# Performance work log

Measured on AMD Instinct MI355X. Metric: run time of the kernel, lower is better.

Reference implementation:

```python
import jax, jax.numpy as jnp
import numpy as np

N = 100_000   # nodes
E = 1_600_000 # edges (avg degree 16)
B = 512       # graphs in batch
F_IN = 64; H = 4; D = 64; HD = H * D; EXTRA = 16
NEG_SLOPE = 0.2  # DGL GATConv default


def _gat_conv(x, src, dst, W, al, ar, bias):
    """DGL GATConv: fc -> per-head attn logits -> edge leaky_relu -> segment softmax over dst -> scatter-sum."""
    h = (x @ W).reshape(N, H, D)                       # [N,H,D]
    el = jnp.sum(h * al, axis=-1)                      # [N,H]
    er = jnp.sum(h * ar, axis=-1)                      # [N,H]
    e = jax.nn.leaky_relu(el[src] + er[dst], NEG_SLOPE)  # [E,H]
    m = jax.ops.segment_max(e, dst, num_segments=N)    # [N,H]
    m = jnp.where(jnp.isfinite(m), m, 0.0)             # guard empty segments
    ex = jnp.exp(e - m[dst])                           # [E,H]
    den = jax.ops.segment_sum(ex, dst, num_segments=N) # [N,H]
    alpha = ex / jnp.maximum(den[dst], 1e-9)           # [E,H]
    msg = h[src] * alpha[:, :, None]                   # [E,H,D]
    out = jax.ops.segment_sum(msg, dst, num_segments=N) + bias.reshape(1, H, D)
    return out  # [N,H,D]


def setup_inputs() -> dict:
    key = jax.random.key(0)
    ks = jax.random.split(key, 26)
    nrm = lambda k, shape: jax.random.normal(k, shape, dtype=jnp.float32) * 0.5
    src = jax.random.randint(ks[0], (E,), 0, N)
    # ensure every node has >=1 incoming edge (DGL disallows zero in-degree by default)
    dst = jnp.concatenate([jnp.arange(N), jax.random.randint(ks[1], (E - N,), 0, N)])
    node_graph = jnp.sort(jax.random.randint(ks[2], (N,), 0, B))
    inp = dict(
        src=src, dst=dst, node_graph=node_graph,
        feats_node=jax.random.normal(ks[3], (N, F_IN), dtype=jnp.float32),
        feats_graph=jax.random.normal(ks[4], (B, EXTRA), dtype=jnp.float32),
        W1=nrm(ks[5], (F_IN, HD)), al1=nrm(ks[6], (H, D)), ar1=nrm(ks[7], (H, D)), bg1=jnp.zeros(HD),
        W2=nrm(ks[8], (HD, HD)),  al2=nrm(ks[9], (H, D)), ar2=nrm(ks[10], (H, D)), bg2=jnp.zeros(HD),
        W3=nrm(ks[11], (HD, HD)), al3=nrm(ks[12], (H, D)), ar3=nrm(ks[13], (H, D)), bg3=jnp.zeros(HD),
        sw=nrm(ks[14], (HD, 1)), sb=jnp.zeros(1),
        lw1=nrm(ks[15], (HD + EXTRA, 2 * D)), lb1=jnp.zeros(2 * D),
        lw2=nrm(ks[16], (2 * D, D)), lb2=jnp.zeros(D),
        lw3=nrm(ks[17], (D, 1)), lb3=jnp.zeros(1),
    )
    return inp


def reference(src, dst, node_graph, feats_node, feats_graph,
              W1, al1, ar1, bg1, W2, al2, ar2, bg2, W3, al3, ar3, bg3,
              sw, sb, lw1, lb1, lw2, lb2, lw3, lb3):
    selu = jax.nn.selu
    x = selu(_gat_conv(feats_node, src, dst, W1, al1, ar1, bg1)).reshape(N, HD)
    x = selu(_gat_conv(x, src, dst, W2, al2, ar2, bg2)).reshape(N, HD)
    x = selu(_gat_conv(x, src, dst, W3, al3, ar3, bg3)).reshape(N, HD)
    # WeightedAverage readout: sigmoid-scored weighted mean per graph
    w = jax.nn.sigmoid(x @ sw + sb)                               # [N,1]
    num = jax.ops.segment_sum(w * x, node_graph, num_segments=B)  # [B,HD]
    den = jax.ops.segment_sum(w, node_graph, num_segments=B)      # [B,1]
    emb = num / jnp.maximum(den, 1e-9)
    y = jnp.concatenate([emb, feats_graph], axis=1)
    y = selu(y @ lw1 + lb1)
    y = selu(y @ lw2 + lb2)
    return y @ lw3 + lb3  # [B,1]
```

## Files before the change

kernel.cpp:

```cpp
#include <hip/hip_runtime.h>

#define N_NODES 100000
#define N_EDGES 1600000
#define N_GRAPHS 512
#define F_IN 64
#define HD 256
#define EXTRA 16
#define SCAN_BLOCK 512

typedef float f32x4 __attribute__((ext_vector_type(4)));
typedef _Float16 f16x4 __attribute__((ext_vector_type(4)));
typedef _Float16 f16x8 __attribute__((ext_vector_type(8)));

__device__ __forceinline__ float selu_f(float x) {
    const float a = 1.6732632423543772f, sc = 1.0507009873554805f;
    return x > 0.f ? sc * x : sc * a * (__expf(x) - 1.f);
}

__global__ __launch_bounds__(256) void hist_k(const int* __restrict__ dst, int* __restrict__ hist) {
    int j = blockIdx.x * 256 + threadIdx.x;
    if (j < N_EDGES) atomicAdd(&hist[dst[j]], 1);
}

__global__ __launch_bounds__(SCAN_BLOCK) void scan1_k(const int* __restrict__ hist,
                                                      int* __restrict__ row_ptr,
                                                      int* __restrict__ bsums) {
    __shared__ int sm[SCAN_BLOCK];
    int t = threadIdx.x;
    int i = blockIdx.x * SCAN_BLOCK + t;
    int v = (i < N_NODES) ? hist[i] : 0;
    sm[t] = v;
    __syncthreads();
    for (int off = 1; off < SCAN_BLOCK; off <<= 1) {
        int add = (t >= off) ? sm[t - off] : 0;
        __syncthreads();
        sm[t] += add;
        __syncthreads();
    }
    if (i < N_NODES) row_ptr[i] = sm[t] - v;
    if (t == SCAN_BLOCK - 1) bsums[blockIdx.x] = sm[t];
}

__global__ __launch_bounds__(256) void scan23_k(int* __restrict__ row_ptr, const int* __restrict__ bsums,
                                                int* __restrict__ cursor, int nb) {
    __shared__ int bs[256];
    int t = threadIdx.x;
    bs[t] = (t < nb) ? bsums[t] : 0;
    __syncthreads();
    for (int off = 1; off < 256; off <<= 1) {
        int add = (t >= off) ? bs[t - off] : 0;
        __syncthreads();
        bs[t] += add;
        __syncthreads();
    }
    int i = blockIdx.x * 256 + t;
    if (i < N_NODES) {
        int b = i / SCAN_BLOCK;
        int p = b > 0 ? bs[b - 1] : 0;
        int r = row_ptr[i] + p;
        row_ptr[i] = r;
        cursor[i] = r;
    }
    if (i == 0) row_ptr[N_NODES] = N_EDGES;
}

__global__ __launch_bounds__(256) void scatter_k(const int* __restrict__ src,
                                                 const int* __restrict__ dst,
                                                 int* __restrict__ cursor,
                                                 int* __restrict__ csr_src) {
    int j = blockIdx.x * 256 + threadIdx.x;
    if (j < N_EDGES) {
        int r = atomicAdd(&cursor[dst[j]], 1);
        r = r < N_EDGES ? r : N_EDGES - 1;
        csr_src[r] = src[j];
    }
}

__device__ __forceinline__ void wsplit(const float* __restrict__ W, _Float16* __restrict__ Wh,
                                       _Float16* __restrict__ Wl, int idx, int K) {
    int n = idx / K, k = idx - n * K;
    float w = W[(size_t)k * HD + n];
    _Float16 hi = (_Float16)w;
    Wh[idx] = hi;
    Wl[idx] = (_Float16)(w - (float)hi);
}

__global__ __launch_bounds__(256) void prep_k(const float* __restrict__ W1,
                                              const float* __restrict__ W2,
                                              const float* __restrict__ W3,
                                              _Float16* __restrict__ W1h, _Float16* __restrict__ W1l,
                                              _Float16* __restrict__ W2h, _Float16* __restrict__ W2l,
                                              _Float16* __restrict__ W3h, _Float16* __restrict__ W3l,
                                              const int* __restrict__ node_graph,
                                              int* __restrict__ gstart) {
    int b = blockIdx.x, t = threadIdx.x;
    if (b < 64) {
        wsplit(W1, W1h, W1l, b * 256 + t, F_IN);
    } else if (b < 320) {
        wsplit(W2, W2h, W2l, (b - 64) * 256 + t, HD);
    } else if (b < 576) {
        wsplit(W3, W3h, W3l, (b - 320) * 256 + t, HD);
    } else {
        int g = (b - 576) * 256 + t;
        if (g > N_GRAPHS) return;
        int lo = 0, hi = N_NODES;
        while (lo < hi) {
            int mid = (lo + hi) >> 1;
            if (node_graph[mid] < g) lo = mid + 1; else hi = mid;
        }
        gstart[g] = lo;
    }
}

template <int K, bool F32A, int ATERMS>
__global__ __launch_bounds__(256) void gemm_split_k(const void* __restrict__ Aptr,
                                                    const _Float16* __restrict__ Alo_p,
                                                    const _Float16* __restrict__ Bt_hi,
                                                    const _Float16* __restrict__ Bt_lo,
                                                    const float* __restrict__ al,
                                                    const float* __restrict__ ar,
                                                    _Float16* __restrict__ Chi,
                                                    float* __restrict__ el,
                                                    float* __restrict__ er, int M) {
    const int BM = 64, BN = 128, LDP = 40;
    __shared__ union {
        struct {
            _Float16 Ash[BM][LDP];
            _Float16 Asl[BM][LDP];
            _Float16 Bsh[BN][LDP];
            _Float16 Bsl[BN][LDP];
        } s;
        _Float16 ctile[BM][BN];
    } u;
    __shared__ float pl[4][64];
    __shared__ float pr[4][64];
    _Float16 (&Ash)[BM][LDP] = u.s.Ash;
    _Float16 (&Asl)[BM][LDP] = u.s.Asl;
    _Float16 (&Bsh)[BN][LDP] = u.s.Bsh;
    _Float16 (&Bsl)[BN][LDP] = u.s.Bsl;

    int tid = threadIdx.x;
    int w = tid >> 6, lane = tid & 63;
    int q = lane >> 4, l16 = lane & 15;
    int row0 = blockIdx.y * BM, col0 = blockIdx.x * BN;
    f32x4 acc[4][2] = {};

    int ar_ = tid >> 2, ao = (tid & 3) * 8;
    f16x8 rAh, rAl, rBh[2], rBl[2];

    auto load_tile = [&](int k0) {
        int gr = row0 + ar_;
        if constexpr (F32A) {
            const float* A32 = (const float*)Aptr;
            float vv[8] = {};
            if (gr < M) {
                float4 va = *(const float4*)(A32 + (size_t)gr * K + k0 + ao);
                float4 vb = *(const float4*)(A32 + (size_t)gr * K + k0 + ao + 4);
                vv[0] = va.x; vv[1] = va.y; vv[2] = va.z; vv[3] = va.w;
                vv[4] = vb.x; vv[5] = vb.y; vv[6] = vb.z; vv[7] = vb.w;
            }
            f16x8 h, l;
#pragma unroll
            for (int i = 0; i < 8; i++) {
                h[i] = (_Float16)vv[i];
                l[i] = (_Float16)(vv[i] - (float)h[i]);
            }
            rAh = h; rAl = l;
        } else {
            const _Float16* Ahi = (const _Float16*)Aptr;
            f16x8 vh = {};
            if (gr < M) {
                vh = *(const f16x8*)(Ahi + (size_t)gr * K + k0 + ao);
                if constexpr (ATERMS == 3) rAl = *(const f16x8*)(Alo_p + (size_t)gr * K + k0 + ao);
            } else if constexpr (ATERMS == 3) {
                rAl = f16x8{};
            }
            rAh = vh;
        }
#pragma unroll
        for (int c = 0; c < 2; c++) {
            int cc = tid + c * 256;
            int br = cc >> 2, bo = (cc & 3) * 8;
            int gb = col0 + br;
            rBh[c] = *(const f16x8*)(Bt_hi + (size_t)gb * K + k0 + bo);
            rBl[c] = *(const f16x8*)(Bt_lo + (size_t)gb * K + k0 + bo);
        }
    };
    auto store_tile = [&]() {
        *(f16x8*)&Ash[ar_][ao] = rAh;
        if constexpr (ATERMS == 3) *(f16x8*)&Asl[ar_][ao] = rAl;
#pragma unroll
        for (int c = 0; c < 2; c++) {
            int cc = tid + c * 256;
            int br = cc >> 2, bo = (cc & 3) * 8;
            *(f16x8*)&Bsh[br][bo] = rBh[c];
            *(f16x8*)&Bsl[br][bo] = rBl[c];
        }
    };

    load_tile(0);
    store_tile();
    __syncthreads();

    for (int k0 = 0; k0 < K; k0 += 32) {
        bool more = (k0 + 32) < K;
        if (more) load_tile(k0 + 32);

        f16x8 ah[4], alo2[4], bh[2], bl[2];
#pragma unroll
        for (int mf = 0; mf < 4; mf++) {
            int m = mf * 16 + l16;
            ah[mf] = *(const f16x8*)&Ash[m][q * 8];
            if constexpr (ATERMS == 3) alo2[mf] = *(const f16x8*)&Asl[m][q * 8];
        }
#pragma unroll
        for (int nf = 0; nf < 2; nf++) {
            int n = w * 32 + nf * 16 + l16;
            bh[nf] = *(const f16x8*)&Bsh[n][q * 8];
            bl[nf] = *(const f16x8*)&Bsl[n][q * 8];
        }
#pragma unroll
        for (int mf = 0; mf < 4; mf++)
#pragma unroll
            for (int nf = 0; nf < 2; nf++) {
                acc[mf][nf] = __builtin_amdgcn_mfma_f32_16x16x32_f16(ah[mf], bh[nf], acc[mf][nf], 0, 0, 0);
                acc[mf][nf] = __builtin_amdgcn_mfma_f32_16x16x32_f16(ah[mf], bl[nf], acc[mf][nf], 0, 0, 0);
                if constexpr (ATERMS == 3)
                    acc[mf][nf] = __builtin_amdgcn_mfma_f32_16x16x32_f16(alo2[mf], bh[nf], acc[mf][nf], 0, 0, 0);
            }
        if (more) {
            __syncthreads();
            store_tile();
            __syncthreads();
        }
    }

    __syncthreads();

    const int hh = (col0 >> 6) + (w >> 1);
    float alv[2], arv[2];
#pragma unroll
    for (int nf = 0; nf < 2; nf++) {
        int d = (w & 1) * 32 + nf * 16 + l16;
        alv[nf] = al[hh * 64 + d];
        arv[nf] = ar[hh * 64 + d];
    }
#pragma unroll
    for (int mf = 0; mf < 4; mf++) {
#pragma unroll
        for (int i = 0; i < 4; i++) {
            int rl = mf * 16 + q * 4 + i;
            float e_l = 0.f, e_r = 0.f;
#pragma unroll
            for (int nf = 0; nf < 2; nf++) {
                float v = acc[mf][nf][i];
                u.ctile[rl][w * 32 + nf * 16 + l16] = (_Float16)v;
                e_l = fmaf(v, alv[nf], e_l);
                e_r = fmaf(v, arv[nf], e_r);
            }
#pragma unroll
            for (int off = 1; off < 16; off <<= 1) {
                e_l += __shfl_xor(e_l, off, 64);
                e_r += __shfl_xor(e_r, off, 64);
            }
            if (l16 == 0) {
                pl[w][rl] = e_l;
                pr[w][rl] = e_r;
            }
        }
    }
    __syncthreads();
#pragma unroll
    for (int j = 0; j < 4; j++) {
        int c = tid + j * 256;
        int rr2 = c >> 4, co = (c & 15) * 8;
        int gr = row0 + rr2;
        if (gr < M)
            *(f16x8*)(Chi + (size_t)gr * HD + col0 + co) = *(const f16x8*)&u.ctile[rr2][co];
    }
    int h2 = (tid >> 6) & 1, rr = tid & 63;
    int grow = row0 + rr;
    if (grow < M) {
        if (tid < 128) el[(size_t)grow * 4 + (col0 >> 6) + h2] = pl[2 * h2][rr] + pl[2 * h2 + 1][rr];
        else           er[(size_t)grow * 4 + (col0 >> 6) + h2] = pr[2 * h2][rr] + pr[2 * h2 + 1][rr];
    }
}

template <int OUT>
__global__ __launch_bounds__(256) void gat_aggregate_k(const _Float16* __restrict__ hb,
                                                       const float* __restrict__ el,
                                                       const float* __restrict__ er,
                                                       const int* __restrict__ csr_src,
                                                       const int* __restrict__ row_ptr,
                                                       const float* __restrict__ bias,
                                                       _Float16* __restrict__ xhi,
                                                       const float* __restrict__ sw,
                                                       const float* __restrict__ sb,
                                                       float* __restrict__ wsc) {
    __shared__ float wlds[4][64][4];
    __shared__ int snlds[4][64];
    int wv = threadIdx.x >> 6;
    int lane = threadIdx.x & 63;
    int v = blockIdx.x * 4 + wv;
    bool valid = v < N_NODES;
    int vc = valid ? v : 0;
    int rs = row_ptr[vc];
    int deg = valid ? row_ptr[vc + 1] - rs : 0;
    float4 erv = make_float4(0.f, 0.f, 0.f, 0.f);
    if (valid) erv = *(const float4*)(er + (size_t)vc * 4);

    const int eo = lane >> 5;
    const int fl = lane & 31;
    const int headf = fl >> 3;

    float a[8] = {};
    float dw = 0.f;
    float m_h = 0.f, er_h = 0.f;

    if (deg <= 64) {
        float e0 = -1e30f, e1 = -1e30f, e2 = -1e30f, e3 = -1e30f;
        int my_sn = 0;
        if (lane < deg) {
            my_sn = csr_src[rs + lane];
            float4 elv = *(const float4*)(el + (size_t)my_sn * 4);
            float t0 = elv.x + erv.x, t1 = elv.y + erv.y, t2 = elv.z + erv.z, t3 = elv.w + erv.w;
            e0 = t0 > 0.f ? t0 : 0.2f * t0;
            e1 = t1 > 0.f ? t1 : 0.2f * t1;
            e2 = t2 > 0.f ? t2 : 0.2f * t2;
            e3 = t3 > 0.f ? t3 : 0.2f * t3;
        }
        int P = (deg + 1) >> 1;
        f16x8 hv[8];
        int pA = P < 4 ? P : 4;
#pragma unroll
        for (int u = 0; u < 4; u++) {
            if (u < pA) {
                int idx = 2 * u + eo;
                int cidx = idx < deg ? idx : deg - 1;
                int snb = __shfl(my_sn, cidx, 64);
                hv[u] = *(const f16x8*)(hb + (size_t)snb * HD + fl * 8);
            }
        }
        float m0 = e0, m1 = e1, m2 = e2, m3 = e3;
        for (int off = 1; off < deg; off <<= 1) {
            m0 = fmaxf(m0, __shfl_xor(m0, off, 64));
            m1 = fmaxf(m1, __shfl_xor(m1, off, 64));
            m2 = fmaxf(m2, __shfl_xor(m2, off, 64));
            m3 = fmaxf(m3, __shfl_xor(m3, off, 64));
        }
        if (lane < deg) {
            wlds[wv][lane][0] = __expf(e0 - m0);
            wlds[wv][lane][1] = __expf(e1 - m1);
            wlds[wv][lane][2] = __expf(e2 - m2);
            wlds[wv][lane][3] = __expf(e3 - m3);
            snlds[wv][lane] = my_sn;
        }

        int pB = P < 8 ? P : 8;
#pragma unroll
        for (int u = 4; u < 8; u++) {
            if (u < pB) {
                int idx = 2 * u + eo;
                int cidx = idx < deg ? idx : deg - 1;
                hv[u] = *(const f16x8*)(hb + (size_t)snlds[wv][cidx] * HD + fl * 8);
            }
        }
        for (int pb = 0; pb < P; pb += 8) {
#pragma unroll
            for (int j = 0; j < 8; j++) {
                int p = pb + j;
                if (p >= P) break;
                int idx = 2 * p + eo;
                float w = (idx < deg) ? wlds[wv][idx][headf] : 0.f;
                dw += w;
                f16x8 h = hv[j];
#pragma unroll
                for (int i = 0; i < 8; i++) a[i] = fmaf(w, (float)h[i], a[i]);
                int pn = p + 8;
                if (pn < P) {
                    int idx2 = 2 * pn + eo;
                    int cidx2 = idx2 < deg ? idx2 : deg - 1;
                    hv[j] = *(const f16x8*)(hb + (size_t)snlds[wv][cidx2] * HD + fl * 8);
                }
            }
        }
    } else {
        float m[4] = {-1e30f, -1e30f, -1e30f, -1e30f};
        float s[4] = {0.f, 0.f, 0.f, 0.f};
        for (int t = lane; t < deg; t += 64) {
            int sn = csr_src[rs + t];
            float4 elv = *(const float4*)(el + (size_t)sn * 4);
            float e[4];
            e[0] = elv.x + erv.x; e[1] = elv.y + erv.y; e[2] = elv.z + erv.z; e[3] = elv.w + erv.w;
#pragma unroll
            for (int hh = 0; hh < 4; hh++) {
                float ev = e[hh] > 0.f ? e[hh] : 0.2f * e[hh];
                float mn = fmaxf(m[hh], ev);
                s[hh] = s[hh] * __expf(m[hh] - mn) + __expf(ev - mn);
                m[hh] = mn;
            }
        }
#pragma unroll
        for (int off = 32; off >= 1; off >>= 1) {
#pragma unroll
            for (int hh = 0; hh < 4; hh++) {
                float mo = __shfl_xor(m[hh], off, 64);
                float so = __shfl_xor(s[hh], off, 64);
                float mn = fmaxf(m[hh], mo);
                s[hh] = s[hh] * __expf(m[hh] - mn) + so * __expf(mo - mn);
                m[hh] = mn;
            }
        }
        m_h = headf == 0 ? m[0] : headf == 1 ? m[1] : headf == 2 ? m[2] : m[3];
        float dh = headf == 0 ? s[0] : headf == 1 ? s[1] : headf == 2 ? s[2] : s[3];
        er_h = headf == 0 ? erv.x : headf == 1 ? erv.y : headf == 2 ? erv.z : erv.w;
        dw = (eo == 0) ? dh : 0.f;

        for (int t = 0; t < deg; t += 2) {
            int idx = t + eo;
            int cidx = idx < deg ? idx : idx - 1;
            int sn = csr_src[rs + cidx];
            float w = 0.f;
            if (idx < deg) {
                float e = el[(size_t)sn * 4 + headf] + er_h;
                e = e > 0.f ? e : 0.2f * e;
                w = __expf(e - m_h);
            }
            f16x8 hv = *(const f16x8*)(hb + (size_t)sn * HD + fl * 8);
#pragma unroll
            for (int i = 0; i < 8; i++) a[i] = fmaf(w, (float)hv[i], a[i]);
        }
    }

#pragma unroll
    for (int i = 0; i < 8; i++) a[i] += __shfl_xor(a[i], 32, 64);
    dw += __shfl_xor(dw, 32, 64);
    float inv_den = 1.f / fmaxf(dw, 1e-9f);

    float4 bv0 = *(const float4*)(bias + fl * 8);
    float4 bv1 = *(const float4*)(bias + fl * 8 + 4);
    float o[8];
    o[0] = selu_f(fmaf(a[0], inv_den, bv0.x));
    o[1] = selu_f(fmaf(a[1], inv_den, bv0.y));
    o[2] = selu_f(fmaf(a[2], inv_den, bv0.z));
    o[3] = selu_f(fmaf(a[3], inv_den, bv0.w));
    o[4] = selu_f(fmaf(a[4], inv_den, bv1.x));
    o[5] = selu_f(fmaf(a[5], inv_den, bv1.y));
    o[6] = selu_f(fmaf(a[6], inv_den, bv1.z));
    o[7] = selu_f(fmaf(a[7], inv_den, bv1.w));

    if constexpr (OUT == 0) {
        if (valid && eo == 0) {
            f16x8 oh;
#pragma unroll
            for (int i = 0; i < 8; i++) oh[i] = (_Float16)o[i];
            *(f16x8*)(xhi + (size_t)v * HD + fl * 8) = oh;
        }
    } else {
        float p;
        if (eo == 0) {
            if (valid) {
                f16x4 oh;
                oh.x = (_Float16)o[0]; oh.y = (_Float16)o[1];
                oh.z = (_Float16)o[2]; oh.w = (_Float16)o[3];
                *(f16x4*)(xhi + (size_t)v * HD + fl * 8) = oh;
            }
            float4 sv = *(const float4*)(sw + fl * 8);
            p = o[0] * sv.x + o[1] * sv.y + o[2] * sv.z + o[3] * sv.w;
        } else {
            if (valid) {
                f16x4 oh;
                oh.x = (_Float16)o[4]; oh.y = (_Float16)o[5];
                oh.z = (_Float16)o[6]; oh.w = (_Float16)o[7];
                *(f16x4*)(xhi + (size_t)v * HD + fl * 8 + 4) = oh;
            }
            float4 sv = *(const float4*)(sw + fl * 8 + 4);
            p = o[4] * sv.x + o[5] * sv.y + o[6] * sv.z + o[7] * sv.w;
        }
#pragma unroll
        for (int off = 1; off < 64; off <<= 1) p += __shfl_xor(p, off, 64);
        if (lane == 0 && valid) wsc[v] = 1.f / (1.f + __expf(-(p + sb[0])));
    }
}

__global__ __launch_bounds__(256) void readout_part_k(const _Float16* __restrict__ x,
                                                      const float* __restrict__ wsc,
                                                      const int* __restrict__ gstart,
                                                      float* __restrict__ y0p) {
    int g = blockIdx.x >> 2, c = blockIdx.x & 3;
    int f = threadIdx.x;
    int s0 = gstart[g], e0 = gstart[g + 1];
    int len = e0 - s0;
    int cs = s0 + (len * c) / 4, ce = s0 + (len * (c + 1)) / 4;
    float num = 0.f, den = 0.f;
#pragma unroll 4
    for (int n = cs; n < ce; n++) {
        float wn = wsc[n];
        num = fmaf(wn, (float)x[(size_t)n * HD + f], num);
        den += wn;
    }
    float* dst = y0p + (size_t)(g * 4 + c) * 257;
    dst[f] = num;
    if (f == 0) dst[256] = den;
}

__global__ __launch_bounds__(128) void mlp_k(const float* __restrict__ y0p,
                                             const float* __restrict__ fg,
                                             const float* __restrict__ lw1, const float* __restrict__ lb1,
                                             const float* __restrict__ lw2, const float* __restrict__ lb2,
                                             const float* __restrict__ lw3, const float* __restrict__ lb3,
                                             float* __restrict__ out) {
    __shared__ float y0s[272];
    __shared__ float y1s[128];
    int g = blockIdx.x, t = threadIdx.x;
    const float* p0 = y0p + (size_t)(g * 4 + 0) * 257;
    const float* p1 = y0p + (size_t)(g * 4 + 1) * 257;
    const float* p2 = y0p + (size_t)(g * 4 + 2) * 257;
    const float* p3 = y0p + (size_t)(g * 4 + 3) * 257;
    float den = p0[256] + p1[256] + p2[256] + p3[256];
    float invden = 1.f / fmaxf(den, 1e-9f);
    for (int i = t; i < 256; i += 128)
        y0s[i] = (p0[i] + p1[i] + p2[i] + p3[i]) * invden;
    if (t < EXTRA) y0s[256 + t] = fg[g * EXTRA + t];
    __syncthreads();
    float acc = lb1[t];
    for (int k = 0; k < 272; k++) acc = fmaf(y0s[k], lw1[k * 128 + t], acc);
    y1s[t] = selu_f(acc);
    __syncthreads();
    if (t < 64) {
        float a2 = lb2[t];
        for (int k = 0; k < 128; k++) a2 = fmaf(y1s[k], lw2[k * 64 + t], a2);
        float v2 = selu_f(a2);
        float p = v2 * lw3[t];
#pragma unroll
        for (int off = 1; off < 64; off <<= 1) p += __shfl_xor(p, off, 64);
        if (t == 0) out[g] = p + lb3[0];
    }
}

extern "C" void kernel_launch(void* const* d_in, const int* in_sizes, int n_in,
                              void* d_out, int out_size, void* d_ws, size_t ws_size,
                              hipStream_t stream) {
    const int* src = (const int*)d_in[0];
    const int* dst = (const int*)d_in[1];
    const int* node_graph = (const int*)d_in[2];
    const float* feats_node = (const float*)d_in[3];
    const float* feats_graph = (const float*)d_in[4];
    const float* W1 = (const float*)d_in[5];
    const float* al1 = (const float*)d_in[6];
    const float* ar1 = (const float*)d_in[7];
    const float* bg1 = (const float*)d_in[8];
    const float* W2 = (const float*)d_in[9];
    const float* al2 = (const float*)d_in[10];
    const float* ar2 = (const float*)d_in[11];
    const float* bg2 = (const float*)d_in[12];
    const float* W3 = (const float*)d_in[13];
    const float* al3 = (const float*)d_in[14];
    const float* ar3 = (const float*)d_in[15];
    const float* bg3 = (const float*)d_in[16];
    const float* sw = (const float*)d_in[17];
    const float* sb = (const float*)d_in[18];
    const float* lw1 = (const float*)d_in[19];
    const float* lb1 = (const float*)d_in[20];
    const float* lw2 = (const float*)d_in[21];
    const float* lb2 = (const float*)d_in[22];
    const float* lw3 = (const float*)d_in[23];
    const float* lb3 = (const float*)d_in[24];
    float* out = (float*)d_out;

    char* ws = (char*)d_ws;
    size_t off = 0;
    auto alloc = [&](size_t bytes) -> char* {
        char* p = ws + off;
        off += (bytes + 255) & ~(size_t)255;
        return p;
    };
    _Float16* xhi = (_Float16*)alloc((size_t)N_NODES * HD * 2);
    _Float16* hhi = (_Float16*)alloc((size_t)N_NODES * HD * 2);
    _Float16* W1hi = (_Float16*)alloc((size_t)F_IN * HD * 2);
    _Float16* W1lo = (_Float16*)alloc((size_t)F_IN * HD * 2);
    _Float16* W2hi = (_Float16*)alloc((size_t)HD * HD * 2);
    _Float16* W2lo = (_Float16*)alloc((size_t)HD * HD * 2);
    _Float16* W3hi = (_Float16*)alloc((size_t)HD * HD * 2);
    _Float16* W3lo = (_Float16*)alloc((size_t)HD * HD * 2);
    float* el = (float*)alloc((size_t)N_NODES * 4 * 4);
    float* er = (float*)alloc((size_t)N_NODES * 4 * 4);
    float* wsc = (float*)alloc((size_t)N_NODES * 4);
    float* y0p = (float*)alloc((size_t)N_GRAPHS * 4 * 257 * 4);
    int* hist = (int*)alloc((size_t)N_NODES * 4);
    int* row_ptr = (int*)alloc((size_t)(N_NODES + 1) * 4);
    int* cursor = (int*)alloc((size_t)N_NODES * 4);
    int* csr_src = (int*)alloc((size_t)N_EDGES * 4);
    int* gstart = (int*)alloc((size_t)(N_GRAPHS + 1) * 4);
    int* bsums = (int*)alloc(256 * 4);
    (void)ws_size; (void)in_sizes; (void)n_in; (void)out_size;

    hipMemsetAsync(hist, 0, (size_t)N_NODES * 4, stream);

    hist_k<<<(N_EDGES + 255) / 256, 256, 0, stream>>>(dst, hist);
    int nb = (N_NODES + SCAN_BLOCK - 1) / SCAN_BLOCK;
    scan1_k<<<nb, SCAN_BLOCK, 0, stream>>>(hist, row_ptr, bsums);
    scan23_k<<<(N_NODES + 255) / 256, 256, 0, stream>>>(row_ptr, bsums, cursor, nb);
    scatter_k<<<(N_EDGES + 255) / 256, 256, 0, stream>>>(src, dst, cursor, csr_src);

    prep_k<<<579, 256, 0, stream>>>(W1, W2, W3, W1hi, W1lo, W2hi, W2lo, W3hi, W3lo, node_graph, gstart);

    dim3 ggrid(HD / 128, (N_NODES + 63) / 64);
    int nwb = (N_NODES + 3) / 4;

    gemm_split_k<F_IN, true, 3><<<ggrid, 256, 0, stream>>>((const void*)feats_node, nullptr, W1hi, W1lo, al1, ar1, hhi, el, er, N_NODES);
    gat_aggregate_k<0><<<nwb, 256, 0, stream>>>(hhi, el, er, csr_src, row_ptr, bg1, xhi, nullptr, nullptr, nullptr);
    gemm_split_k<HD, false, 2><<<ggrid, 256, 0, stream>>>((const void*)xhi, nullptr, W2hi, W2lo, al2, ar2, hhi, el, er, N_NODES);
    gat_aggregate_k<0><<<nwb, 256, 0, stream>>>(hhi, el, er, csr_src, row_ptr, bg2, xhi, nullptr, nullptr, nullptr);
    gemm_split_k<HD, false, 2><<<ggrid, 256, 0, stream>>>((const void*)xhi, nullptr, W3hi, W3lo, al3, ar3, hhi, el, er, N_NODES);
    gat_aggregate_k<1><<<nwb, 256, 0, stream>>>(hhi, el, er, csr_src, row_ptr, bg3, xhi, sw, sb, wsc);

    readout_part_k<<<N_GRAPHS * 4, 256, 0, stream>>>(xhi, wsc, gstart, y0p);
    mlp_k<<<N_GRAPHS, 128, 0, stream>>>(y0p, feats_graph, lw1, lb1, lw2, lb2, lw3, lb3, out);
}
```

Measured before the change: 882.8 us.

## Merge CSR build kernels with weight prep and first GEMM via block-range dispatch

The edge histogram is folded into the weight-split/gstart prep kernel, and the CSR scatter is folded into the first-layer GEMM kernel. Each merged kernel decides its role from blockIdx ranges. This removes two launches and lets independent work share the GPU, so the atomic-bound scatter can overlap with the GEMM compute. The risks are that block scheduling order puts the edge blocks first, which limits the overlap, and that the merged kernel's register and LDS usage is set by the GEMM body, which may lower occupancy for the scatter blocks.

Result: slower. 907.9 us (+2.8%).

```diff
diff --git a/kernel.cpp b/kernel.cpp
--- a/kernel.cpp
+++ b/kernel.cpp
@@ -7,6 +7,7 @@
 #define HD 256
 #define EXTRA 16
 #define SCAN_BLOCK 512
+#define EDGE_BLOCKS 6250
 
 typedef float f32x4 __attribute__((ext_vector_type(4)));
 typedef _Float16 f16x4 __attribute__((ext_vector_type(4)));
@@ -15,11 +16,6 @@
 __device__ __forceinline__ float selu_f(float x) {
     const float a = 1.6732632423543772f, sc = 1.0507009873554805f;
     return x > 0.f ? sc * x : sc * a * (__expf(x) - 1.f);
-}
-
-__global__ __launch_bounds__(256) void hist_k(const int* __restrict__ dst, int* __restrict__ hist) {
-    int j = blockIdx.x * 256 + threadIdx.x;
-    if (j < N_EDGES) atomicAdd(&hist[dst[j]], 1);
 }
 
 __global__ __launch_bounds__(SCAN_BLOCK) void scan1_k(const int* __restrict__ hist,
@@ -64,18 +60,6 @@
     if (i == 0) row_ptr[N_NODES] = N_EDGES;
 }
 
-__global__ __launch_bounds__(256) void scatter_k(const int* __restrict__ src,
-                                                 const int* __restrict__ dst,
-                                                 int* __restrict__ cursor,
-                                                 int* __restrict__ csr_src) {
-    int j = blockIdx.x * 256 + threadIdx.x;
-    if (j < N_EDGES) {
-        int r = atomicAdd(&cursor[dst[j]], 1);
-        r = r < N_EDGES ? r : N_EDGES - 1;
-        csr_src[r] = src[j];
-    }
-}
-
 __device__ __forceinline__ void wsplit(const float* __restrict__ W, _Float16* __restrict__ Wh,
                                        _Float16* __restrict__ Wl, int idx, int K) {
     int n = idx / K, k = idx - n * K;
@@ -85,15 +69,22 @@
     Wl[idx] = (_Float16)(w - (float)hi);
 }
 
-__global__ __launch_bounds__(256) void prep_k(const float* __restrict__ W1,
-                                              const float* __restrict__ W2,
-                                              const float* __restrict__ W3,
-                                              _Float16* __restrict__ W1h, _Float16* __restrict__ W1l,
-                                              _Float16* __restrict__ W2h, _Float16* __restrict__ W2l,
-                                              _Float16* __restrict__ W3h, _Float16* __restrict__ W3l,
-                                              const int* __restrict__ node_graph,
-                                              int* __restrict__ gstart) {
-    int b = blockIdx.x, t = threadIdx.x;
+__global__ __launch_bounds__(256) void histprep_k(const int* __restrict__ dst, int* __restrict__ hist,
+                                                  const float* __restrict__ W1,
+                                                  const float* __restrict__ W2,
+                                                  const float* __restrict__ W3,
+                                                  _Float16* __restrict__ W1h, _Float16* __restrict__ W1l,
+                                                  _Float16* __restrict__ W2h, _Float16* __restrict__ W2l,
+                                                  _Float16* __restrict__ W3h, _Float16* __restrict__ W3l,
+                                                  const int* __restrict__ node_graph,
+                                                  int* __restrict__ gstart) {
+    int bid = blockIdx.x, t = threadIdx.x;
+    if (bid < EDGE_BLOCKS) {
+        int j = bid * 256 + t;
+        if (j < N_EDGES) atomicAdd(&hist[dst[j]], 1);
+        return;
+    }
+    int b = bid - EDGE_BLOCKS;
     if (b < 64) {
         wsplit(W1, W1h, W1l, b * 256 + t, F_IN);
     } else if (b < 320) {
@@ -113,17 +104,18 @@
 }
 
 template <int K, bool F32A, int ATERMS>
-__global__ __launch_bounds__(256) void gemm_split_k(const void* __restrict__ Aptr,
-                                                    const _Float16* __restrict__ Alo_p,
-                                                    const _Float16* __restrict__ Bt_hi,
-                                                    const _Float16* __restrict__ Bt_lo,
-                                                    const float* __restrict__ al,
-                                                    const float* __restrict__ ar,
-                                                    _Float16* __restrict__ Chi,
-                                                    float* __restrict__ el,
-                                                    float* __restrict__ er, int M) {
+__device__ __forceinline__ void gemm_body(int bx, int by,
+                                          const void* __restrict__ Aptr,
+                                          const _Float16* __restrict__ Alo_p,
+                                          const _Float16* __restrict__ Bt_hi,
+                                          const _Float16* __restrict__ Bt_lo,
+                                          const float* __restrict__ al,
+                                          const float* __restrict__ ar,
+                                          _Float16* __restrict__ Chi,
+                                          float* __restrict__ el,
+                                          float* __restrict__ er, int M) {
     const int BM = 64, BN = 128, LDP = 40;
-    __shared__ union {
+    __shared__ union U {
         struct {
             _Float16 Ash[BM][LDP];
             _Float16 Asl[BM][LDP];
@@ -142,7 +134,7 @@
     int tid = threadIdx.x;
     int w = tid >> 6, lane = tid & 63;
     int q = lane >> 4, l16 = lane & 15;
-    int row0 = blockIdx.y * BM, col0 = blockIdx.x * BN;
+    int row0 = by * BM, col0 = bx * BN;
     f32x4 acc[4][2] = {};
 
     int ar_ = tid >> 2, ao = (tid & 3) * 8;
@@ -284,6 +276,46 @@
         if (tid < 128) el[(size_t)grow * 4 + (col0 >> 6) + h2] = pl[2 * h2][rr] + pl[2 * h2 + 1][rr];
         else           er[(size_t)grow * 4 + (col0 >> 6) + h2] = pr[2 * h2][rr] + pr[2 * h2 + 1][rr];
     }
+}
+
+template <int K, bool F32A, int ATERMS>
+__global__ __launch_bounds__(256) void gemm_k(const void* __restrict__ Aptr,
+                                              const _Float16* __restrict__ Alo_p,
+                                              const _Float16* __restrict__ Bt_hi,
+                                              const _Float16* __restrict__ Bt_lo,
+                                              const float* __restrict__ al,
+                                              const float* __restrict__ ar,
+                                              _Float16* __restrict__ Chi,
+                                              float* __restrict__ el,
+                                              float* __restrict__ er, int M) {
+    gemm_body<K, F32A, ATERMS>(blockIdx.x, blockIdx.y, Aptr, Alo_p, Bt_hi, Bt_lo, al, ar, Chi, el, er, M);
+}
+
+__global__ __launch_bounds__(256) void mega1_k(const int* __restrict__ src,
+                                               const int* __restrict__ dst,
+                                               int* __restrict__ cursor,
+                                               int* __restrict__ csr_src,
+                                               const float* __restrict__ feats_node,
+                                               const _Float16* __restrict__ W1h,
+                                               const _Float16* __restrict__ W1l,
+                                               const float* __restrict__ al1,
+                                               const float* __restrict__ ar1,
+                                               _Float16* __restrict__ hhi,
+                                               float* __restrict__ el,
+                                               float* __restrict__ er) {
+    int bid = blockIdx.x;
+    if (bid < EDGE_BLOCKS) {
+        int j = bid * 256 + threadIdx.x;
+        if (j < N_EDGES) {
+            int r = atomicAdd(&cursor[dst[j]], 1);
+            r = r < N_EDGES ? r : N_EDGES - 1;
+            csr_src[r] = src[j];
+        }
+        return;
+    }
+    int g = bid - EDGE_BLOCKS;
+    gemm_body<F_IN, true, 3>(g & 1, g >> 1, (const void*)feats_node, nullptr, W1h, W1l,
+                             al1, ar1, hhi, el, er, N_NODES);
 }
 
 template <int OUT>
@@ -597,22 +629,24 @@
 
     hipMemsetAsync(hist, 0, (size_t)N_NODES * 4, stream);
 
-    hist_k<<<(N_EDGES + 255) / 256, 256, 0, stream>>>(dst, hist);
+    histprep_k<<<EDGE_BLOCKS + 579, 256, 0, stream>>>(dst, hist, W1, W2, W3,
+                                                      W1hi, W1lo, W2hi, W2lo, W3hi, W3lo,
+                                                      node_graph, gstart);
     int nb = (N_NODES + SCAN_BLOCK - 1) / SCAN_BLOCK;
     scan1_k<<<nb, SCAN_BLOCK, 0, stream>>>(hist, row_ptr, bsums);
     scan23_k<<<(N_NODES + 255) / 256, 256, 0, stream>>>(row_ptr, bsums, cursor, nb);
-    scatter_k<<<(N_EDGES + 255) / 256, 256, 0, stream>>>(src, dst, cursor, csr_src);
-
-    prep_k<<<579, 256, 0, stream>>>(W1, W2, W3, W1hi, W1lo, W2hi, W2lo, W3hi, W3lo, node_graph, gstart);
 
     dim3 ggrid(HD / 128, (N_NODES + 63) / 64);
+    int g1blocks = (HD / 128) * ((N_NODES + 63) / 64);
     int nwb = (N_NODES + 3) / 4;
 
-    gemm_split_k<F_IN, true, 3><<<ggrid, 256, 0, stream>>>((const void*)feats_node, nullptr, W1hi, W1lo, al1, ar1, hhi, el, er, N_NODES);
+    mega1_k<<<EDGE_BLOCKS + g1blocks, 256, 0, stream>>>(src, dst, cursor, csr_src,
+                                                        feats_node, W1hi, W1lo, al1, ar1,
+                                                        hhi, el, er);
     gat_aggregate_k<0><<<nwb, 256, 0, stream>>>(hhi, el, er, csr_src, row_ptr, bg1, xhi, nullptr, nullptr, nullptr);
-    gemm_split_k<HD, false, 2><<<ggrid, 256, 0, stream>>>((const void*)xhi, nullptr, W2hi, W2lo, al2, ar2, hhi, el, er, N_NODES);
+    gemm_k<HD, false, 2><<<ggrid, 256, 0, stream>>>((const void*)xhi, nullptr, W2hi, W2lo, al2, ar2, hhi, el, er, N_NODES);
     gat_aggregate_k<0><<<nwb, 256, 0, stream>>>(hhi, el, er, csr_src, row_ptr, bg2, xhi, nullptr, nullptr, nullptr);
-    gemm_split_k<HD, false, 2><<<ggrid, 256, 0, stream>>>((const void*)xhi, nullptr, W3hi, W3lo, al3, ar3, hhi, el, er, N_NODES);
+    gemm_k<HD, false, 2><<<ggrid, 256, 0, stream>>>((const void*)xhi, nullptr, W3hi, W3lo, al3, ar3, hhi, el, er, N_NODES);
     gat_aggregate_k<1><<<nwb, 256, 0, stream>>>(hhi, el, er, csr_src, row_ptr, bg3, xhi, sw, sb, wsc);
 
     readout_part_k<<<N_GRAPHS * 4, 256, 0, stream>>>(xhi, wsc, gstart, y0p);
```
